# Optimization experiments

Measured on AMD Instinct MI355X. Metric: run time of the kernel, lower is better.

## Reference

```python
import jax, jax.numpy as jnp
import numpy as np

NEG_INF = -1e30  # log-semiring zero
B, T, D, V, L = 16, 800, 512, 5000, 100


def setup_inputs() -> dict:
    key = jax.random.key(0)
    k1, k2, k3, k4, k5, k6 = jax.random.split(key, 6)
    hs_pad = jax.random.normal(k1, (B, T, D), dtype=jnp.float32)
    W = jax.random.normal(k2, (D, V), dtype=jnp.float32) / np.sqrt(D)
    b = jnp.zeros((V,), dtype=jnp.float32)
    hlens = jax.random.randint(k3, (B,), T // 2, T + 1, dtype=jnp.int32)
    labels = jax.random.randint(k4, (B, L), 1, V, dtype=jnp.int32)  # blank=0 excluded
    label_lens = jax.random.randint(k5, (B,), L // 2, L + 1, dtype=jnp.int32)
    return {"hs_pad": hs_pad, "W": W, "b": b, "hlens": hlens,
            "labels": labels, "label_lens": label_lens}


def _ctc_tot_scores(log_probs, hlens, labels, label_lens):
    # Standard CTC log-semiring forward DP (equivalent to k2 CTC-topology
    # intersect_dense + get_tot_scores). log_probs: [B,T,V], blank id = 0.
    Bb, Tt, Vv = log_probs.shape
    Ll = labels.shape[1]
    S = 2 * Ll + 1  # extended sequence: blank, l1, blank, l2, ..., blank
    ext = jnp.zeros((Bb, S), dtype=labels.dtype).at[:, 1::2].set(labels)
    # skip transition (s-2 -> s) allowed iff ext[s] != blank and ext[s] != ext[s-2]
    skip = jnp.concatenate(
        [jnp.zeros((Bb, 2), dtype=bool),
         (ext[:, 2:] != ext[:, :-2]) & (ext[:, 2:] != 0)], axis=1)
    # emissions along extended labels: lp_ext[b,t,s] = log_probs[b,t,ext[b,s]]
    lp_ext = jax.vmap(lambda lp, e: lp[:, e])(log_probs, ext)  # [B,T,S]
    alpha = jnp.full((Bb, S), NEG_INF, dtype=log_probs.dtype)
    alpha = alpha.at[:, 0].set(lp_ext[:, 0, 0])
    alpha = alpha.at[:, 1].set(lp_ext[:, 0, 1])

    def step(alpha, inp):
        t, lp_t = inp  # lp_t: [B,S]
        prev1 = jnp.pad(alpha[:, :-1], ((0, 0), (1, 0)), constant_values=NEG_INF)
        prev2 = jnp.pad(alpha[:, :-2], ((0, 0), (2, 0)), constant_values=NEG_INF)
        prev2 = jnp.where(skip, prev2, NEG_INF)
        a = jnp.logaddexp(jnp.logaddexp(alpha, prev1), prev2) + lp_t
        # freeze rows whose sequence has ended (t >= hlen)
        return jnp.where((t < hlens)[:, None], a, alpha), None

    ts = jnp.arange(1, Tt)
    alpha, _ = jax.lax.scan(step, alpha, (ts, jnp.swapaxes(lp_ext, 0, 1)[1:]))
    last = 2 * label_lens  # index of final blank per utterance
    a_last = jnp.take_along_axis(alpha, last[:, None], axis=1)[:, 0]
    a_prev = jnp.take_along_axis(alpha, (last - 1)[:, None], axis=1)[:, 0]
    return jnp.logaddexp(a_last, a_prev)  # [B] total log-likelihoods


def reference(hs_pad, W, b, hlens, labels, label_lens):
    # ctc_lo Linear (dropout_rate=0 -> identity) + log_softmax
    logits = jnp.einsum('btd,dv->btv', hs_pad, W) + b
    log_probs = jax.nn.log_softmax(logits, axis=-1)
    tot = _ctc_tot_scores(log_probs, hlens, labels, label_lens)
    # forward_scores = -tot_scores, reduce=True -> mean
    return jnp.mean(-tot)
```

## Files before the change

### kernel.cpp

```cpp
#include <hip/hip_runtime.h>

#define NEG_INF -1e30f

typedef __attribute__((ext_vector_type(8))) __bf16 bf16x8;
typedef __attribute__((ext_vector_type(4))) float f32x4;

constexpr int Bb = 16, T = 800, D = 512, V = 5000, L = 100;
constexpr int ROWS = Bb * T;
constexpr int S = 2 * L + 1;
constexpr int SP = 208;
constexpr int VP = 5120;
constexpr int NCB = VP / 128;
constexpr int NRB = ROWS / 128;
constexpr int NGB = Bb * 50;
constexpr int CONVB = ROWS * D / 1024;
constexpr int RSTRIDE = SP * 4;

static __device__ __forceinline__ unsigned short f2bf(float x) {
  union { float f; unsigned u; } v; v.f = x;
  unsigned r = (v.u + 0x7FFFu + ((v.u >> 16) & 1u)) >> 16;
  return (unsigned short)r;
}

static __device__ __forceinline__ double dpp_shr1_zero_d(double x) {
  long long b = __double_as_longlong(x);
  int lo = (int)(b & 0xFFFFFFFFLL);
  int hi = (int)(b >> 32);
  int nlo = __builtin_amdgcn_update_dpp(0, lo, 0x138, 0xF, 0xF, false);
  int nhi = __builtin_amdgcn_update_dpp(0, hi, 0x138, 0xF, 0xF, false);
  return __longlong_as_double(((long long)(unsigned)nlo) | ((long long)nhi << 32));
}

static __device__ __forceinline__ float ex2(float x) { return __builtin_amdgcn_exp2f(x); }
static __device__ __forceinline__ float lg2(float x) { return __builtin_amdgcn_logf(x); }

static __device__ __forceinline__ float lg2d(double z) {
  long long b = __double_as_longlong(z);
  int e = (int)((b >> 52) & 0x7FF);
  if (e == 0) return -1.0e30f;
  unsigned mant = (unsigned)((b >> 29) & 0x7FFFFFu);
  float mf = __int_as_float(0x3F800000u | mant);
  return (float)(e - 1023) + lg2(mf);
}

__global__ __launch_bounds__(256) void k_prep(const float* __restrict__ hs,
                                              const float* __restrict__ W,
                                              unsigned short* __restrict__ A,
                                              unsigned short* __restrict__ Wt) {
  __shared__ float tile[64][65];
  int blk = blockIdx.x;
  if (blk < CONVB) {
    int i = blk * 256 + threadIdx.x;
    float4 f = ((const float4*)hs)[i];
    ushort4 o;
    o.x = f2bf(f.x); o.y = f2bf(f.y); o.z = f2bf(f.z); o.w = f2bf(f.w);
    ((ushort4*)A)[i] = o;
    return;
  }
  int g = blk - CONVB;
  int v0 = (g % (VP / 64)) * 64, k0 = (g / (VP / 64)) * 64;
  int tl = threadIdx.x & 63, th = threadIdx.x >> 6;
#pragma unroll
  for (int i = 0; i < 16; i++) {
    int k = k0 + th + i * 4;
    int v = v0 + tl;
    tile[th + i * 4][tl] = (v < V) ? W[(size_t)k * V + v] : 0.f;
  }
  __syncthreads();
#pragma unroll
  for (int i = 0; i < 16; i++) {
    int v = v0 + th + i * 4;
    int k = k0 + tl;
    Wt[(size_t)v * D + k] = f2bf(tile[tl][th + i * 4]);
  }
}

__global__ __launch_bounds__(256) void k_gather(const unsigned short* __restrict__ A,
                                                const unsigned short* __restrict__ Wt,
                                                const float* __restrict__ bias,
                                                const int* __restrict__ labels,
                                                float* __restrict__ glog) {
  int tid = threadIdx.x;
  int lane = tid & 63, w = tid >> 6;
  int q = lane >> 4, c = lane & 15;
  int b = blockIdx.x & 15, chk = blockIdx.x >> 4;
  int t0 = chk * 16;
  int bT = b * T, bL = b * L;
  int st0 = (w == 0) ? 0 : 4 + (w - 1) * 3;
  int nst = (w == 0) ? 4 : 3;

  int evs[4]; float bvs[4];
#pragma unroll
  for (int j = 0; j < 4; j++) {
    int st = st0 + (j < nst ? j : nst - 1);
    int s = st * 16 + c;
    evs[j] = (s < S && (s & 1)) ? labels[bL + (s >> 1)] : 0;
    bvs[j] = bias[evs[j]];
  }
  const unsigned short* Arow = A + (size_t)(bT + t0 + c) * D;
  f32x4 acc[4];
#pragma unroll
  for (int j = 0; j < 4; j++) acc[j] = (f32x4){0.f, 0.f, 0.f, 0.f};
  for (int kk = 0; kk < D; kk += 32) {
    bf16x8 aa = *(const bf16x8*)(Arow + kk + q * 8);
#pragma unroll
    for (int j = 0; j < 4; j++) {
      bf16x8 bb = *(const bf16x8*)(Wt + (size_t)evs[j] * D + kk + q * 8);
      acc[j] = __builtin_amdgcn_mfma_f32_16x16x32_bf16(aa, bb, acc[j], 0, 0, 0);
    }
  }
#pragma unroll
  for (int j = 0; j < 4; j++) {
    if (j >= nst) break;
    int st = st0 + j;
#pragma unroll
    for (int r = 0; r < 4; r++)
      glog[(size_t)(bT + t0 + q * 4 + r) * SP + st * 16 + c] = acc[j][r] + bvs[j];
  }
}

__global__ __launch_bounds__(256) void k_fused(const unsigned short* __restrict__ A,
                                               const unsigned short* __restrict__ Wt,
                                               const float* __restrict__ bias,
                                               const float* __restrict__ glog,
                                               const int* __restrict__ labels,
                                               const int* __restrict__ hlens,
                                               const int* __restrict__ llens,
                                               float* __restrict__ partM,
                                               float* __restrict__ partS,
                                               float* __restrict__ rawtot) {
  __shared__ unsigned short As[128 * 64];
  __shared__ unsigned short Bs[128 * 64];
  __shared__ float redM[2][128];
  __shared__ float redS[2][128];

  int blk = blockIdx.x;
  if (blk < Bb) {
    if (threadIdx.x >= 64) return;
    int b = blk, l = threadIdx.x;
    int col4 = ((4 * l < SP) ? 4 * l : SP - 4) * 4;
    const char* rp = (const char*)glog + (size_t)b * T * RSTRIDE + col4;
    int hl = hlens[b];

    int i0 = (2 * l < L) ? 2 * l : L - 1;
    int i1 = (2 * l + 1 < L) ? 2 * l + 1 : L - 1;
    int im = (l >= 1) ? 2 * l - 1 : 0; im = im < L ? im : L - 1;
    int lab0 = labels[b * L + i0];
    int lab1 = labels[b * L + i1];
    int labm = labels[b * L + im];
    bool sk1 = (l >= 1) && (lab0 != 0) && (lab0 != labm);
    bool sk3 = (lab1 != 0) && (lab1 != lab0);

    constexpr float LOG2E = 1.44269504f;
    f32x4 g0 = *(const f32x4*)rp;
    double z0 = (l == 0) ? 1.0 : 0.0;
    double z1 = (l == 0) ? (double)ex2((g0.y - g0.x) * LOG2E) : 0.0;
    double z2 = 0.0, z3 = 0.0;
    double Csum = (double)g0.x;
    int Kc = 0;

    constexpr int PF = 8;
    const char* p = rp + RSTRIDE;
    f32x4 buf[PF];
#pragma unroll
    for (int j = 0; j < PF; j++) { buf[j] = *(const f32x4*)p; p += RSTRIDE; }

#define DP_STEPZ(G) {                                                  \
    double e1 = (double)ex2(((G).y - (G).x) * LOG2E);                  \
    double e3 = (double)ex2(((G).w - (G).x) * LOG2E);                  \
    Csum += (double)(G).x;                                             \
    double p3 = dpp_shr1_zero_d(z3);                                   \
    double nz0 = z0 + p3;                                              \
    double nz1 = (z1 + z0 + (sk1 ? p3 : 0.0)) * e1;                    \
    double nz2 = z2 + z1;                                              \
    double nz3 = (z3 + z2 + (sk3 ? z1 : 0.0)) * e3;                    \
    z0 = nz0; z1 = nz1; z2 = nz2; z3 = nz3; }

    int t = 1;
    for (; t + PF <= hl; t += PF) {
#pragma unroll
      for (int j = 0; j < PF; j++) {
        f32x4 G = buf[j];
        buf[j] = *(const f32x4*)p;
        if (t + j + PF < hl - 1) p += RSTRIDE;
        DP_STEPZ(G)
      }
      long long bz0 = __double_as_longlong(z0), bz1 = __double_as_longlong(z1);
      long long bz2 = __double_as_longlong(z2), bz3 = __double_as_longlong(z3);
      int e0 = (int)((bz0 >> 52) & 0x7FF), e1i = (int)((bz1 >> 52) & 0x7FF);
      int e2i = (int)((bz2 >> 52) & 0x7FF), e3i = (int)((bz3 >> 52) & 0x7FF);
      int em = e0 > e1i ? e0 : e1i;
      em = em > e2i ? em : e2i;
      em = em > e3i ? em : e3i;
#pragma unroll
      for (int o = 1; o < 64; o <<= 1) { int q2 = __shfl_xor(em, o); em = em > q2 ? em : q2; }
      if (em > 0 && em < 2046) {
        double sc = __longlong_as_double((long long)(2046 - em) << 52);
        z0 *= sc; z1 *= sc; z2 *= sc; z3 *= sc;
        Kc += em - 1023;
      }
    }
    {
      int rem = hl - t;
#pragma unroll
      for (int j = 0; j < PF; j++) {
        if (j < rem) { f32x4 G = buf[j]; DP_STEPZ(G) }
      }
    }
#undef DP_STEPZ

    int ll = llens[b];
    int s1i = 2 * ll, s2i = 2 * ll - 1;
    int c1 = s1i & 3, c2 = s2i & 3;
    float lz0 = lg2d(z0), lz1 = lg2d(z1), lz2 = lg2d(z2), lz3 = lg2d(z3);
    float cand1 = c1 == 0 ? lz0 : c1 == 1 ? lz1 : c1 == 2 ? lz2 : lz3;
    float cand2 = c2 == 0 ? lz0 : c2 == 1 ? lz1 : c2 == 2 ? lz2 : lz3;
    float v1 = __shfl(cand1, s1i >> 2);
    float v2 = __shfl(cand2, s2i >> 2);
    if (l == 0) {
      float m = fmaxf(v1, v2);
      float d = m + lg2(ex2(v1 - m) + ex2(v2 - m));
      rawtot[b] = (float)(Csum + 0.6931471805599453 * ((double)Kc + (double)d));
    }
    return;
  }

  int gblk = blk - Bb;
  int cb = gblk % NCB, rb = gblk / NCB;
  int tid = threadIdx.x;
  int lane = tid & 63, w = tid >> 6;
  int q = lane >> 4, c = lane & 15;
  int mh = w & 1, nh = w >> 1;
  int row0 = rb * 128, n0 = cb * 128;
  int lr = lane >> 3, lc = lane & 7;
  int oc = (lc ^ lr) * 8;

  f32x4 acc[4][4];
#pragma unroll
  for (int mt = 0; mt < 4; mt++)
#pragma unroll
    for (int nt = 0; nt < 4; nt++) acc[mt][nt] = (f32x4){0.f, 0.f, 0.f, 0.f};

  for (int kk = 0; kk < D; kk += 64) {
#pragma unroll
    for (int j = 0; j < 4; j++) {
      int i = w * 4 + j;
      const unsigned short* ga = A + (size_t)(row0 + i * 8 + lr) * D + kk + oc;
      __builtin_amdgcn_global_load_lds(
          (const __attribute__((address_space(1))) void*)ga,
          (__attribute__((address_space(3))) void*)(As + i * 512), 16, 0, 0);
      const unsigned short* gb = Wt + (size_t)(n0 + i * 8 + lr) * D + kk + oc;
      __builtin_amdgcn_global_load_lds(
          (const __attribute__((address_space(1))) void*)gb,
          (__attribute__((address_space(3))) void*)(Bs + i * 512), 16, 0, 0);
    }
    __syncthreads();
#pragma unroll
    for (int kq = 0; kq < 2; kq++) {
      int o = ((kq * 4 + q) ^ (c & 7)) * 8;
      bf16x8 af[4], bfr[4];
#pragma unroll
      for (int mt = 0; mt < 4; mt++)
        af[mt] = *(const bf16x8*)(As + (mh * 64 + mt * 16 + c) * 64 + o);
#pragma unroll
      for (int nt = 0; nt < 4; nt++)
        bfr[nt] = *(const bf16x8*)(Bs + (nh * 64 + nt * 16 + c) * 64 + o);
#pragma unroll
      for (int mt = 0; mt < 4; mt++)
#pragma unroll
        for (int nt = 0; nt < 4; nt++)
          acc[mt][nt] = __builtin_amdgcn_mfma_f32_16x16x32_bf16(af[mt], bfr[nt], acc[mt][nt], 0, 0, 0);
    }
    __syncthreads();
  }

  int vcb[4]; float bv[4];
#pragma unroll
  for (int nt = 0; nt < 4; nt++) {
    vcb[nt] = n0 + nh * 64 + nt * 16 + c;
    bv[nt] = (vcb[nt] < V) ? bias[vcb[nt]] : 0.f;
  }
#pragma unroll
  for (int mt = 0; mt < 4; mt++) {
#pragma unroll
    for (int r = 0; r < 4; r++) {
      float x[4]; float m = NEG_INF;
#pragma unroll
      for (int nt = 0; nt < 4; nt++) {
        x[nt] = (vcb[nt] < V) ? (acc[mt][nt][r] + bv[nt]) : NEG_INF;
        m = fmaxf(m, x[nt]);
      }
#pragma unroll
      for (int o = 1; o < 16; o <<= 1) m = fmaxf(m, __shfl_xor(m, o));
      float s = 0.f;
#pragma unroll
      for (int nt = 0; nt < 4; nt++) s += __expf(x[nt] - m);
#pragma unroll
      for (int o = 1; o < 16; o <<= 1) s += __shfl_xor(s, o);
      if (c == 0) {
        int rloc = mh * 64 + mt * 16 + q * 4 + r;
        redM[nh][rloc] = m;
        redS[nh][rloc] = s;
      }
    }
  }
  __syncthreads();
  if (tid < 128) {
    float m0 = redM[0][tid], m1 = redM[1][tid];
    float mm = fmaxf(m0, m1);
    float ss = redS[0][tid] * __expf(m0 - mm) + redS[1][tid] * __expf(m1 - mm);
    partM[(size_t)cb * ROWS + row0 + tid] = mm;
    partS[(size_t)cb * ROWS + row0 + tid] = ss;
  }
}

__global__ __launch_bounds__(256) void k_lse(const float* __restrict__ pM,
                                             const float* __restrict__ pS,
                                             float* __restrict__ lse) {
  int row = blockIdx.x * 256 + threadIdx.x;
  float m = pM[row], s = pS[row];
  for (int cb = 1; cb < NCB; cb++) {
    float M2 = pM[(size_t)cb * ROWS + row], S2 = pS[(size_t)cb * ROWS + row];
    float mn = fmaxf(m, M2);
    s = s * __expf(m - mn) + S2 * __expf(M2 - mn);
    m = mn;
  }
  lse[row] = m + __logf(s);
}

__global__ __launch_bounds__(1024) void k_final(const float* __restrict__ lse,
                                                const float* __restrict__ rawtot,
                                                const int* __restrict__ hlens,
                                                float* __restrict__ out) {
  __shared__ float acc[Bb];
  int w = threadIdx.x >> 6, l = threadIdx.x & 63;
  int hl = hlens[w];
  float s = 0.f;
  for (int t = l; t < hl; t += 64) s += lse[w * T + t];
#pragma unroll
  for (int o = 1; o < 64; o <<= 1) s += __shfl_xor(s, o);
  if (l == 0) acc[w] = rawtot[w] - s;
  __syncthreads();
  if (threadIdx.x == 0) {
    float m = 0.f;
    for (int i = 0; i < Bb; i++) m += acc[i];
    out[0] = -m / (float)Bb;
  }
}

extern "C" void kernel_launch(void* const* d_in, const int* in_sizes, int n_in,
                              void* d_out, int out_size, void* d_ws, size_t ws_size,
                              hipStream_t stream) {
  const float* hs    = (const float*)d_in[0];
  const float* W     = (const float*)d_in[1];
  const float* bias  = (const float*)d_in[2];
  const int* hlens   = (const int*)d_in[3];
  const int* labels  = (const int*)d_in[4];
  const int* llens   = (const int*)d_in[5];
  float* out = (float*)d_out;

  char* ws = (char*)d_ws;
  unsigned short* A    = (unsigned short*)(ws);
  unsigned short* Wt   = (unsigned short*)(ws + 13107200);
  float*          partM= (float*)(ws + 18350080);
  float*          partS= (float*)(ws + 20398080);
  float*          lse  = (float*)(ws + 22446080);
  float*          glog = (float*)(ws + 22497280);
  float*          rawtot=(float*)(ws + 33146880);

  k_prep<<<CONVB + (VP / 64) * (D / 64), 256, 0, stream>>>(hs, W, A, Wt);
  k_gather<<<NGB, 256, 0, stream>>>(A, Wt, bias, labels, glog);
  k_fused<<<Bb + NCB * NRB, 256, 0, stream>>>(A, Wt, bias, glog, labels, hlens, llens,
                                              partM, partS, rawtot);
  k_lse<<<ROWS / 256, 256, 0, stream>>>(partM, partS, lse);
  k_final<<<1, 1024, 0, stream>>>(lse, rawtot, hlens, out);

  (void)in_sizes; (void)n_in; (void)out_size; (void)ws_size;
}
```

Measured before the change: 281.7 us.

## Stage CTC emission rows into LDS via async global_load_lds double buffering

The CTC DP blocks now copy chunks of 16 timesteps of emissions from global memory into a double-buffered LDS region using global_load_lds. Two chunks stay in flight while the DP consumes the current one. This replaces the per-lane 8-deep register prefetch of scattered 16-byte loads, with the aim of hiding global latency on the serial DP critical path. Shared memory is now a single raw buffer aliased between the GEMM tiles and the DP staging. The change relies on hand-written vmcnt and lgkmcnt waits being exactly right, and the renormalisation interval becomes 16 steps.

```diff
diff --git a/kernel.cpp b/kernel.cpp
--- a/kernel.cpp
+++ b/kernel.cpp
@@ -15,6 +15,8 @@
 constexpr int NGB = Bb * 50;
 constexpr int CONVB = ROWS * D / 1024;
 constexpr int RSTRIDE = SP * 4;
+constexpr int CH = 16;
+constexpr int CHB = CH * RSTRIDE;
 
 static __device__ __forceinline__ unsigned short f2bf(float x) {
   union { float f; unsigned u; } v; v.f = x;
@@ -129,18 +131,30 @@
                                                float* __restrict__ partM,
                                                float* __restrict__ partS,
                                                float* __restrict__ rawtot) {
-  __shared__ unsigned short As[128 * 64];
-  __shared__ unsigned short Bs[128 * 64];
-  __shared__ float redM[2][128];
-  __shared__ float redS[2][128];
+  __shared__ __attribute__((aligned(16))) char smem[34816];
 
   int blk = blockIdx.x;
   if (blk < Bb) {
     if (threadIdx.x >= 64) return;
     int b = blk, l = threadIdx.x;
     int col4 = ((4 * l < SP) ? 4 * l : SP - 4) * 4;
-    const char* rp = (const char*)glog + (size_t)b * T * RSTRIDE + col4;
+    const char* gvb = (const char*)glog + (size_t)b * T * RSTRIDE;
     int hl = hlens[b];
+    int nch = (hl - 1 + CH - 1) / CH;
+    const size_t gmax = (size_t)T * RSTRIDE - 16;
+
+    auto stage = [&](int cc, int dst) {
+      size_t sb = (size_t)(1 + cc * CH) * RSTRIDE;
+#pragma unroll
+      for (int pg = 0; pg < 13; pg++) {
+        size_t ob = sb + (size_t)pg * 1024 + (size_t)l * 16;
+        if (ob > gmax) ob = gmax;
+        __builtin_amdgcn_global_load_lds(
+            (const __attribute__((address_space(1))) void*)(gvb + ob),
+            (__attribute__((address_space(3))) void*)(smem + dst * CHB + pg * 1024),
+            16, 0, 0);
+      }
+    };
 
     int i0 = (2 * l < L) ? 2 * l : L - 1;
     int i1 = (2 * l + 1 < L) ? 2 * l + 1 : L - 1;
@@ -152,18 +166,15 @@
     bool sk3 = (lab1 != 0) && (lab1 != lab0);
 
     constexpr float LOG2E = 1.44269504f;
-    f32x4 g0 = *(const f32x4*)rp;
+    f32x4 g0 = *(const f32x4*)(gvb + col4);
     double z0 = (l == 0) ? 1.0 : 0.0;
     double z1 = (l == 0) ? (double)ex2((g0.y - g0.x) * LOG2E) : 0.0;
     double z2 = 0.0, z3 = 0.0;
     double Csum = (double)g0.x;
     int Kc = 0;
 
-    constexpr int PF = 8;
-    const char* p = rp + RSTRIDE;
-    f32x4 buf[PF];
-#pragma unroll
-    for (int j = 0; j < PF; j++) { buf[j] = *(const f32x4*)p; p += RSTRIDE; }
+    stage(0, 0);
+    stage(1, 1);
 
 #define DP_STEPZ(G) {                                                  \
     double e1 = (double)ex2(((G).y - (G).x) * LOG2E);                  \
@@ -176,35 +187,42 @@
     double nz3 = (z3 + z2 + (sk3 ? z1 : 0.0)) * e3;                    \
     z0 = nz0; z1 = nz1; z2 = nz2; z3 = nz3; }
 
-    int t = 1;
-    for (; t + PF <= hl; t += PF) {
-#pragma unroll
-      for (int j = 0; j < PF; j++) {
-        f32x4 G = buf[j];
-        buf[j] = *(const f32x4*)p;
-        if (t + j + PF < hl - 1) p += RSTRIDE;
-        DP_STEPZ(G)
+    for (int c = 0; c < nch; ++c) {
+      int cur = c & 1;
+      if (c + 2 < nch) { asm volatile("s_waitcnt vmcnt(13)" ::: "memory"); }
+      else             { asm volatile("s_waitcnt vmcnt(0)"  ::: "memory"); }
+      __builtin_amdgcn_sched_barrier(0);
+      const char* bufc = smem + cur * CHB + col4;
+      int steps = hl - 1 - c * CH; if (steps > CH) steps = CH;
+      if (steps == CH) {
+#pragma unroll
+        for (int j = 0; j < CH; j++) {
+          f32x4 G = *(const f32x4*)(bufc + j * RSTRIDE);
+          DP_STEPZ(G)
+        }
+        long long bz0 = __double_as_longlong(z0), bz1 = __double_as_longlong(z1);
+        long long bz2 = __double_as_longlong(z2), bz3 = __double_as_longlong(z3);
+        int e0 = (int)((bz0 >> 52) & 0x7FF), e1i = (int)((bz1 >> 52) & 0x7FF);
+        int e2i = (int)((bz2 >> 52) & 0x7FF), e3i = (int)((bz3 >> 52) & 0x7FF);
+        int em = e0 > e1i ? e0 : e1i;
+        em = em > e2i ? em : e2i;
+        em = em > e3i ? em : e3i;
+#pragma unroll
+        for (int o = 1; o < 64; o <<= 1) { int q2 = __shfl_xor(em, o); em = em > q2 ? em : q2; }
+        if (em > 0 && em < 2046) {
+          double sc = __longlong_as_double((long long)(2046 - em) << 52);
+          z0 *= sc; z1 *= sc; z2 *= sc; z3 *= sc;
+          Kc += em - 1023;
+        }
+      } else {
+        for (int j = 0; j < steps; j++) {
+          f32x4 G = *(const f32x4*)(bufc + j * RSTRIDE);
+          DP_STEPZ(G)
+        }
       }
-      long long bz0 = __double_as_longlong(z0), bz1 = __double_as_longlong(z1);
-      long long bz2 = __double_as_longlong(z2), bz3 = __double_as_longlong(z3);
-      int e0 = (int)((bz0 >> 52) & 0x7FF), e1i = (int)((bz1 >> 52) & 0x7FF);
-      int e2i = (int)((bz2 >> 52) & 0x7FF), e3i = (int)((bz3 >> 52) & 0x7FF);
-      int em = e0 > e1i ? e0 : e1i;
-      em = em > e2i ? em : e2i;
-      em = em > e3i ? em : e3i;
-#pragma unroll
-      for (int o = 1; o < 64; o <<= 1) { int q2 = __shfl_xor(em, o); em = em > q2 ? em : q2; }
-      if (em > 0 && em < 2046) {
-        double sc = __longlong_as_double((long long)(2046 - em) << 52);
-        z0 *= sc; z1 *= sc; z2 *= sc; z3 *= sc;
-        Kc += em - 1023;
-      }
-    }
-    {
-      int rem = hl - t;
-#pragma unroll
-      for (int j = 0; j < PF; j++) {
-        if (j < rem) { f32x4 G = buf[j]; DP_STEPZ(G) }
+      if (c + 2 < nch) {
+        asm volatile("s_waitcnt lgkmcnt(0)" ::: "memory");
+        stage(c + 2, cur);
       }
     }
 #undef DP_STEPZ
@@ -225,6 +243,11 @@
     return;
   }
 
+  unsigned short* As = (unsigned short*)smem;
+  unsigned short* Bs = (unsigned short*)(smem + 16384);
+  float (*redM)[128] = (float (*)[128])(smem + 32768);
+  float (*redS)[128] = (float (*)[128])(smem + 33792);
+
   int gblk = blk - Bb;
   int cb = gblk % NCB, rb = gblk / NCB;
   int tid = threadIdx.x;
```

Measured after the change: 266.1 us. 5.5% less time.
